# Kernel tuning notes

Hardware: AMD Instinct MI355X
Metric: run time of the kernel (lower is better)

Reference implementation:

```python
import jax, jax.numpy as jnp
import numpy as np

B, H, W = 8, 64, 64
D = 256          # in_dim == key_dim == value_dim
HEADS = 8
DK = D // HEADS  # per-head channels (key == value)
EPS = 1e-5


def _ln(x, g, b):
    m = jnp.mean(x, axis=-1, keepdims=True)
    v = jnp.var(x, axis=-1, keepdims=True)
    return (x - m) * jax.lax.rsqrt(v + EPS) * g + b


def setup_inputs() -> dict:
    key = jax.random.key(0)
    ks = jax.random.split(key, 8)
    return {
        "x1": jax.random.normal(ks[0], (B, H, W, 2 * D), jnp.float32),
        "x2": jax.random.normal(ks[1], (B, H, W, D), jnp.float32),
        "linear_w": jax.random.normal(ks[2], (2 * D, D), jnp.float32) * 0.02,
        "linear_b": jax.random.normal(ks[3], (D,), jnp.float32) * 0.02,
        "ln1_g": jnp.ones((D,), jnp.float32) + jax.random.normal(ks[4], (D,), jnp.float32) * 0.02,
        "ln1_b": jax.random.normal(ks[5], (D,), jnp.float32) * 0.02,
        "reproj_w": jax.random.normal(ks[6], (2 * D, D), jnp.float32) * 0.02,  # 1x1 conv kernel [out,in]
        "reproj_b": jax.random.normal(ks[7], (2 * D,), jnp.float32) * 0.02,
        "ln_attn_g": jnp.ones((2 * D,), jnp.float32),
        "ln_attn_b": jnp.zeros((2 * D,), jnp.float32),
    }


def _cross_attention(n1, n2, reproj_w, reproj_b, ln_g, ln_b):
    # n1 (values source), n2 (keys/queries source): [B,H,W,D]
    N = H * W
    v = n1.reshape(B, N, D).transpose(0, 2, 1).reshape(B, HEADS, DK, N)
    kq = n2.reshape(B, N, D).transpose(0, 2, 1).reshape(B, HEADS, DK, N)
    k = jax.nn.softmax(kq, axis=-1)  # softmax over tokens (dim=2 in torch slice)
    q = jax.nn.softmax(kq, axis=2)   # softmax over per-head channels (dim=1 in torch slice)
    # attended[b,h,d,n] = sum_m sum_e q[b,h,d,m] k[b,h,e,m] v[b,h,e,n]
    ctx = jnp.einsum('bhdm,bhem->bhde', q, k)          # [B,h,dk,dk]
    att = jnp.einsum('bhde,bhen->bhdn', ctx, v)        # [B,h,dk,N]
    agg = att.reshape(B, D, H, W)                      # concat heads along channels
    rep = jnp.einsum('od,bdhw->bohw', reproj_w, agg) + reproj_b[None, :, None, None]
    rep = rep.transpose(0, 2, 3, 1)                    # [B,H,W,2D]
    return _ln(rep, ln_g, ln_b)


def reference(x1, x2, linear_w, linear_b, ln1_g, ln1_b, reproj_w, reproj_b, ln_attn_g, ln_attn_b):
    n1 = _ln(x1 @ linear_w + linear_b, ln1_g, ln1_b)   # [B,H,W,D]
    n2 = _ln(x2, ln1_g, ln1_b)                          # [B,H,W,D]
    attn = _cross_attention(n1, n2, reproj_w, reproj_b, ln_attn_g, ln_attn_b)
    return x1 + attn
```

## Files before the change

kernel.cpp:

```cpp
#include <hip/hip_runtime.h>
#include <stdint.h>

typedef __bf16 bf16x8 __attribute__((ext_vector_type(8)));
typedef float f32x4 __attribute__((ext_vector_type(4)));

#define EPS 1e-5f

#define WAITVM(N) asm volatile("s_waitcnt vmcnt(" #N ")" ::: "memory")
#define WAITLGKM0 asm volatile("s_waitcnt lgkmcnt(0)" ::: "memory")

__device__ __forceinline__ void gl16(const void* g, void* l) {
    __builtin_amdgcn_global_load_lds(
        (const __attribute__((address_space(1))) unsigned int*)g,
        (__attribute__((address_space(3))) unsigned int*)l, 16, 0, 0);
}

__device__ __forceinline__ float b2f(unsigned short u) {
    union { unsigned int i; float f; } c; c.i = ((unsigned int)u) << 16; return c.f;
}
__device__ __forceinline__ unsigned short f2b(float f) {
    union { float f; unsigned int i; } c; c.f = f;
    unsigned int i = c.i;
    return (unsigned short)((i + 0x7FFFu + ((i >> 16) & 1u)) >> 16);
}

__global__ void k_zero(float* __restrict__ p, int n) {
    int i = blockIdx.x * 256 + threadIdx.x;
    if (i < n) p[i] = 0.0f;
}

__global__ void k_params(const float* __restrict__ lw, const float* __restrict__ rw,
                         const float* __restrict__ lb, const float* __restrict__ g1,
                         const float* __restrict__ b1, const float* __restrict__ rb,
                         const float* __restrict__ ga, const float* __restrict__ ba,
                         unsigned short* __restrict__ wt1,
                         unsigned short* __restrict__ rwb,
                         unsigned short* __restrict__ vec) {
    int gid = blockIdx.x * 256 + threadIdx.x;
    if (gid < 131072) {
        int k = gid >> 8, n = gid & 255;
        wt1[((size_t)(k >> 3) * 256 + n) * 8 + (k & 7)] = f2b(lw[gid]);
    } else if (gid < 262144) {
        int j = gid - 131072;
        rwb[j] = f2b(rw[j]);
    } else if (gid < 264448) {
        int j = gid - 262144;
        if (j < 256)       vec[j] = f2b(lb[j]);
        else if (j < 512)  vec[j] = f2b(g1[j - 256]);
        else if (j < 768)  vec[j] = f2b(b1[j - 512]);
        else if (j < 1280) vec[j] = f2b(rb[j - 768]);
        else if (j < 1792) vec[j] = f2b(ga[j - 1280]);
        else               vec[j] = f2b(ba[j - 1792]);
    }
}

__global__ __launch_bounds__(256) void k_stats(const float* __restrict__ x2,
                                               float2* __restrict__ stats) {
    int t = threadIdx.x, lane = t & 63, w = t >> 6;
    size_t row = (size_t)blockIdx.x * 4 + w;
    float4 f = *(const float4*)(x2 + row * 256 + lane * 4);
    float s = f.x + f.y + f.z + f.w;
    float q = f.x * f.x + f.y * f.y + f.z * f.z + f.w * f.w;
#pragma unroll
    for (int msk = 1; msk < 64; msk <<= 1) {
        s += __shfl_xor(s, msk, 64);
        q += __shfl_xor(q, msk, 64);
    }
    float mn = s * (1.0f / 256.0f);
    float rstd = rsqrtf(q * (1.0f / 256.0f) - mn * mn + EPS);
    if (lane == 0) stats[row] = make_float2(mn, rstd);
}

__global__ __launch_bounds__(256) void k_ctx(const float* __restrict__ x2,
                                             const float2* __restrict__ stats,
                                             const unsigned short* __restrict__ vec,
                                             float* __restrict__ ctxraw) {
    __shared__ float E[64 * 36];
    __shared__ float Q[64 * 36];
    __shared__ float gs[32], bs[32];
    int bh = blockIdx.x >> 3;
    int b = bh >> 3, h = bh & 7;
    int ch = blockIdx.x & 7;
    int t = threadIdx.x;
    if (t < 32) { gs[t] = b2f(vec[256 + h * 32 + t]); bs[t] = b2f(vec[512 + h * 32 + t]); }
    __syncthreads();
    int d = t >> 3, e0 = (t & 7) * 4;
    float a0 = 0.f, a1 = 0.f, a2 = 0.f, a3 = 0.f;
    const float* base = x2 + ((size_t)b * 4096 + ch * 512) * 256 + h * 32;
    int srow = b * 4096 + ch * 512;
    const int m = t >> 2, c0 = (t & 3) * 8;
    for (int s0 = 0; s0 < 512; s0 += 64) {
        float2 st = stats[srow + s0 + m];
        const float4* p = (const float4*)(base + (size_t)(s0 + m) * 256 + c0);
        float4 f0 = p[0], f1 = p[1];
        float ev[8];
        ev[0] = __expf((f0.x - st.x) * st.y * gs[c0 + 0] + bs[c0 + 0]);
        ev[1] = __expf((f0.y - st.x) * st.y * gs[c0 + 1] + bs[c0 + 1]);
        ev[2] = __expf((f0.z - st.x) * st.y * gs[c0 + 2] + bs[c0 + 2]);
        ev[3] = __expf((f0.w - st.x) * st.y * gs[c0 + 3] + bs[c0 + 3]);
        ev[4] = __expf((f1.x - st.x) * st.y * gs[c0 + 4] + bs[c0 + 4]);
        ev[5] = __expf((f1.y - st.x) * st.y * gs[c0 + 5] + bs[c0 + 5]);
        ev[6] = __expf((f1.z - st.x) * st.y * gs[c0 + 6] + bs[c0 + 6]);
        ev[7] = __expf((f1.w - st.x) * st.y * gs[c0 + 7] + bs[c0 + 7]);
        float ps = ev[0] + ev[1] + ev[2] + ev[3] + ev[4] + ev[5] + ev[6] + ev[7];
        ps += __shfl_xor(ps, 1, 64);
        ps += __shfl_xor(ps, 2, 64);
        float qi = 1.0f / ps;
        *(float4*)(E + m * 36 + c0)     = make_float4(ev[0], ev[1], ev[2], ev[3]);
        *(float4*)(E + m * 36 + c0 + 4) = make_float4(ev[4], ev[5], ev[6], ev[7]);
        *(float4*)(Q + m * 36 + c0)     = make_float4(ev[0]*qi, ev[1]*qi, ev[2]*qi, ev[3]*qi);
        *(float4*)(Q + m * 36 + c0 + 4) = make_float4(ev[4]*qi, ev[5]*qi, ev[6]*qi, ev[7]*qi);
        __syncthreads();
#pragma unroll 4
        for (int mm = 0; mm < 64; mm++) {
            float qd = Q[mm * 36 + d];
            float4 e4 = *(const float4*)(E + mm * 36 + e0);
            a0 += qd * e4.x; a1 += qd * e4.y; a2 += qd * e4.z; a3 += qd * e4.w;
        }
        __syncthreads();
    }
    float* dst = ctxraw + ((size_t)bh << 10) + (d << 5) + e0;
    atomicAdd(dst + 0, a0);
    atomicAdd(dst + 1, a1);
    atomicAdd(dst + 2, a2);
    atomicAdd(dst + 3, a3);
}

__global__ __launch_bounds__(256) void k_w2(const float* __restrict__ ctxraw,
                                            const unsigned short* __restrict__ rwb,
                                            unsigned short* __restrict__ w2t) {
    __shared__ float ctx_s[1024];
    __shared__ float cinv[32];
    int blk = blockIdx.x;
    int b = blk >> 6, h = (blk >> 3) & 7, os = blk & 7;
    int bh = b * 8 + h;
    int t = threadIdx.x;
#pragma unroll
    for (int i = 0; i < 4; i++) ctx_s[t + 256 * i] = ctxraw[((size_t)bh << 10) + t + 256 * i];
    __syncthreads();
    if (t < 32) {
        float s = 0.f;
#pragma unroll
        for (int d = 0; d < 32; d++) s += ctx_s[d * 32 + t];
        cinv[t] = 1.0f / s;
    }
    __syncthreads();
    int o = os * 64 + (t >> 2);
    int e0 = (t & 3) * 8;
    float wv[32];
    const uint4* wp = (const uint4*)(rwb + (size_t)o * 256 + h * 32);
#pragma unroll
    for (int qd = 0; qd < 4; qd++) {
        uint4 u = wp[qd];
        unsigned int uu[4] = {u.x, u.y, u.z, u.w};
#pragma unroll
        for (int j = 0; j < 4; j++) {
            wv[qd * 8 + j * 2]     = b2f((unsigned short)(uu[j] & 0xFFFFu));
            wv[qd * 8 + j * 2 + 1] = b2f((unsigned short)(uu[j] >> 16));
        }
    }
    float s[8];
#pragma unroll
    for (int j = 0; j < 8; j++) s[j] = 0.f;
#pragma unroll 8
    for (int d = 0; d < 32; d++) {
        float w = wv[d];
#pragma unroll
        for (int j = 0; j < 8; j++) s[j] += ctx_s[d * 32 + e0 + j] * w;
    }
    ushort4 o4a, o4b;
    o4a.x = f2b(s[0] * cinv[e0 + 0]); o4a.y = f2b(s[1] * cinv[e0 + 1]);
    o4a.z = f2b(s[2] * cinv[e0 + 2]); o4a.w = f2b(s[3] * cinv[e0 + 3]);
    o4b.x = f2b(s[4] * cinv[e0 + 4]); o4b.y = f2b(s[5] * cinv[e0 + 5]);
    o4b.z = f2b(s[6] * cinv[e0 + 6]); o4b.w = f2b(s[7] * cinv[e0 + 7]);
    int kb = h * 4 + (e0 >> 3);
    unsigned short* dst = w2t + (size_t)b * 131072 + ((size_t)kb * 512 + o) * 8;
    *(ushort4*)dst = o4a;
    *(ushort4*)(dst + 4) = o4b;
}

__global__ __launch_bounds__(256) void k_gemm1(
    const float* __restrict__ x1, const unsigned short* __restrict__ wt1,
    const unsigned short* __restrict__ vec, unsigned short* __restrict__ n1) {
    __shared__ __align__(16) char pool[33792];
    const int t = threadIdx.x;
    const int lane = t & 63, w = t >> 6;
    const int l15 = lane & 15, quad = lane >> 4;
    const int rb = blockIdx.x;
    const int row0 = rb * 64;
    const int mrow = (w << 4) + l15;

    const float* xrow = x1 + (size_t)(row0 + mrow) * 512 + quad * 8;

    f32x4 acc[16];
#pragma unroll
    for (int i = 0; i < 16; i++) acc[i] = (f32x4){0.f, 0.f, 0.f, 0.f};

    float4 fa[2][2];
    fa[0][0] = *(const float4*)(xrow);
    fa[0][1] = *(const float4*)(xrow + 4);
#pragma unroll
    for (int i = 0; i < 4; i++)
        gl16((const char*)wt1 + (w * 4 + i) * 1024 + lane * 16,
             pool + (w * 4 + i) * 1024);

#pragma unroll
    for (int s = 0; s < 16; ++s) {
        const int cur = s & 1;
        if (s < 15) {
            const float* xn = xrow + (s + 1) * 32;
            fa[cur ^ 1][0] = *(const float4*)xn;
            fa[cur ^ 1][1] = *(const float4*)(xn + 4);
#pragma unroll
            for (int i = 0; i < 4; i++)
                gl16((const char*)wt1 + (size_t)(s + 1) * 16384 + (w * 4 + i) * 1024 + lane * 16,
                     pool + (cur ^ 1) * 16384 + (w * 4 + i) * 1024);
        }
        bf16x8 af;
        af[0] = (__bf16)fa[cur][0].x; af[1] = (__bf16)fa[cur][0].y;
        af[2] = (__bf16)fa[cur][0].z; af[3] = (__bf16)fa[cur][0].w;
        af[4] = (__bf16)fa[cur][1].x; af[5] = (__bf16)fa[cur][1].y;
        af[6] = (__bf16)fa[cur][1].z; af[7] = (__bf16)fa[cur][1].w;
        if (s < 15) { WAITVM(6); } else { WAITVM(0); }
        __builtin_amdgcn_s_barrier();
        const char* Bc = pool + cur * 16384 + quad * 4096 + l15 * 16;
#pragma unroll
        for (int cb = 0; cb < 16; cb++) {
            bf16x8 bf = *(const bf16x8*)(Bc + cb * 256);
            acc[cb] = __builtin_amdgcn_mfma_f32_16x16x32_bf16(af, bf, acc[cb], 0, 0, 0);
        }
        WAITLGKM0;
        __builtin_amdgcn_s_barrier();
    }
#pragma unroll
    for (int cb = 0; cb < 16; cb++) {
        float bc = b2f(vec[(cb << 4) + l15]);
#pragma unroll
        for (int r = 0; r < 4; r++) acc[cb][r] += bc;
    }
    float mean_[4], rstd_[4];
#pragma unroll
    for (int r = 0; r < 4; r++) {
        float s = 0.f, q = 0.f;
#pragma unroll
        for (int cb = 0; cb < 16; cb++) { float v = acc[cb][r]; s += v; q += v * v; }
#pragma unroll
        for (int msk = 1; msk < 16; msk <<= 1) {
            s += __shfl_xor(s, msk, 64);
            q += __shfl_xor(q, msk, 64);
        }
        float mn = s * (1.0f / 256.0f);
        mean_[r] = mn;
        rstd_[r] = rsqrtf(q * (1.0f / 256.0f) - mn * mn + EPS);
    }
    unsigned short* n1s = (unsigned short*)pool;
#pragma unroll
    for (int cb = 0; cb < 16; cb++) {
        int col = (cb << 4) + l15;
        float gg = b2f(vec[256 + col]), bbv = b2f(vec[512 + col]);
#pragma unroll
        for (int r = 0; r < 4; r++) {
            int rr = (w << 4) + (quad << 2) + r;
            n1s[rr * 264 + col] = f2b((acc[cb][r] - mean_[r]) * rstd_[r] * gg + bbv);
        }
    }
    WAITLGKM0;
    __builtin_amdgcn_s_barrier();
    {
        int r = t >> 2;
        const unsigned short* src = n1s + r * 264;
        unsigned short* dst = n1 + (size_t)rb * 16384 + r * 8;
#pragma unroll
        for (int j = 0; j < 8; j++) {
            int chunk = (t & 3) * 8 + j;
            *(uint4*)(dst + chunk * 512) = *(const uint4*)(src + chunk * 8);
        }
    }
}

__global__ __launch_bounds__(512) void k_gemm2(
    const unsigned short* __restrict__ n1, const unsigned short* __restrict__ w2t,
    const unsigned short* __restrict__ vec, const float* __restrict__ x1,
    float* __restrict__ out) {
    __shared__ __align__(16) char pool[66560];
    __shared__ float2 red2[128];
    const int t = threadIdx.x;
    const int lane = t & 63, w = t >> 6;
    const int l15 = lane & 15, quad = lane >> 4;
    const int hf = w >> 2, wr = w & 3;
    const int rb = blockIdx.x;
    const int row0 = rb * 64;
    const char* wb = (const char*)w2t + (size_t)(rb >> 6) * 262144;
    const char* an = (const char*)n1 + (size_t)rb * 32768 + quad * 1024 + ((wr << 4) + l15) * 16;

    f32x4 acc[16];
#pragma unroll
    for (int i = 0; i < 16; i++) acc[i] = (f32x4){0.f, 0.f, 0.f, 0.f};

    bf16x8 areg[2];
    areg[0] = *(const bf16x8*)(an);
#pragma unroll
    for (int i = 0; i < 4; i++)
        gl16(wb + (w * 4 + i) * 1024 + lane * 16, pool + (w * 4 + i) * 1024);

#pragma unroll
    for (int s = 0; s < 8; ++s) {
        const int cur = s & 1;
        if (s < 7) {
            areg[cur ^ 1] = *(const bf16x8*)(an + (s + 1) * 4096);
#pragma unroll
            for (int i = 0; i < 4; i++)
                gl16(wb + (size_t)(s + 1) * 32768 + (w * 4 + i) * 1024 + lane * 16,
                     pool + (cur ^ 1) * 32768 + (w * 4 + i) * 1024);
            WAITVM(5);
        } else {
            WAITVM(0);
        }
        __builtin_amdgcn_s_barrier();
        const char* Bc = pool + cur * 32768 + quad * 8192 + hf * 4096 + l15 * 16;
#pragma unroll
        for (int cb = 0; cb < 16; cb++) {
            bf16x8 bf = *(const bf16x8*)(Bc + cb * 256);
            acc[cb] = __builtin_amdgcn_mfma_f32_16x16x32_bf16(areg[cur], bf, acc[cb], 0, 0, 0);
        }
        WAITLGKM0;
        __builtin_amdgcn_s_barrier();
    }
#pragma unroll
    for (int cb = 0; cb < 16; cb++) {
        float bc = b2f(vec[768 + (hf << 8) + (cb << 4) + l15]);
#pragma unroll
        for (int r = 0; r < 4; r++) acc[cb][r] += bc;
    }
#pragma unroll
    for (int r = 0; r < 4; r++) {
        float s = 0.f, q = 0.f;
#pragma unroll
        for (int cb = 0; cb < 16; cb++) { float v = acc[cb][r]; s += v; q += v * v; }
#pragma unroll
        for (int msk = 1; msk < 16; msk <<= 1) {
            s += __shfl_xor(s, msk, 64);
            q += __shfl_xor(q, msk, 64);
        }
        if (l15 == 0) red2[hf * 64 + (wr << 4) + (quad << 2) + r] = make_float2(s, q);
    }
    WAITLGKM0;
    __builtin_amdgcn_s_barrier();
    float mean_[4], rstd_[4];
#pragma unroll
    for (int r = 0; r < 4; r++) {
        int rl = (wr << 4) + (quad << 2) + r;
        float2 cA = red2[rl], cB = red2[64 + rl];
        float s = cA.x + cB.x, q = cA.y + cB.y;
        float mn = s * (1.0f / 512.0f);
        mean_[r] = mn;
        rstd_[r] = rsqrtf(q * (1.0f / 512.0f) - mn * mn + EPS);
    }
    float* rep = (float*)pool;
#pragma unroll
    for (int hv = 0; hv < 2; ++hv) {
        if (hv) __builtin_amdgcn_s_barrier();
        if (hf == hv) {
#pragma unroll
            for (int cb = 0; cb < 16; cb++) {
                int col = (cb << 4) + l15;
                int gcol = (hv << 8) + col;
                float gg = b2f(vec[1280 + gcol]), bbv = b2f(vec[1792 + gcol]);
#pragma unroll
                for (int r = 0; r < 4; r++)
                    rep[((wr << 4) + (quad << 2) + r) * 260 + col] =
                        (acc[cb][r] - mean_[r]) * rstd_[r] * gg + bbv;
            }
        }
        WAITLGKM0;
        __builtin_amdgcn_s_barrier();
        int rr = t >> 4, c0 = (t & 15) << 2;
#pragma unroll
        for (int j = 0; j < 4; j++) {
            int col = c0 + (j << 6);
            float4 v0 = *(const float4*)(rep + rr * 260 + col);
            float4 v1 = *(const float4*)(rep + (rr + 32) * 260 + col);
            size_t g0 = (size_t)(row0 + rr) * 512 + (hv << 8) + col;
            size_t g1 = g0 + (size_t)32 * 512;
            float4 xa = *(const float4*)(x1 + g0);
            float4 xb = *(const float4*)(x1 + g1);
            v0.x += xa.x; v0.y += xa.y; v0.z += xa.z; v0.w += xa.w;
            v1.x += xb.x; v1.y += xb.y; v1.z += xb.z; v1.w += xb.w;
            *(float4*)(out + g0) = v0;
            *(float4*)(out + g1) = v1;
        }
        WAITLGKM0;
    }
}

extern "C" void kernel_launch(void* const* d_in, const int* in_sizes, int n_in,
                              void* d_out, int out_size, void* d_ws, size_t ws_size,
                              hipStream_t stream) {
    const float* x1 = (const float*)d_in[0];
    const float* x2 = (const float*)d_in[1];
    const float* lw = (const float*)d_in[2];
    const float* lb = (const float*)d_in[3];
    const float* g1 = (const float*)d_in[4];
    const float* b1 = (const float*)d_in[5];
    const float* rw = (const float*)d_in[6];
    const float* rb = (const float*)d_in[7];
    const float* ga = (const float*)d_in[8];
    const float* ba = (const float*)d_in[9];
    float* out = (float*)d_out;

    char* ws = (char*)d_ws;
    float*          ctxr  = (float*)(ws);
    float2*         stats = (float2*)(ws + 262144);
    unsigned short* wt1   = (unsigned short*)(ws + 524288);
    unsigned short* rwb   = (unsigned short*)(ws + 786432);
    unsigned short* vec   = (unsigned short*)(ws + 1048576);
    unsigned short* w2t   = (unsigned short*)(ws + 1064960);
    unsigned short* n1    = (unsigned short*)(ws + 4194304);

    k_zero<<<dim3(256), dim3(256), 0, stream>>>(ctxr, 65536);
    k_params<<<dim3(1033), dim3(256), 0, stream>>>(lw, rw, lb, g1, b1, rb, ga, ba,
                                                   wt1, rwb, vec);
    k_stats<<<dim3(8192), dim3(256), 0, stream>>>(x2, stats);
    k_ctx<<<dim3(512), dim3(256), 0, stream>>>(x2, stats, vec, ctxr);
    k_w2<<<dim3(512), dim3(256), 0, stream>>>(ctxr, rwb, w2t);
    k_gemm1<<<dim3(512), dim3(256), 0, stream>>>(x1, wt1, vec, n1);
    k_gemm2<<<dim3(512), dim3(512), 0, stream>>>(n1, w2t, vec, x1, out);
}
```

Before: 234.6 us.

## Fuse linear+LN GEMM with reprojection GEMM into one kernel keeping n1 in LDS

Merges k_gemm1 and k_gemm2 into a single kernel that processes 128 rows per block with 512 threads, keeping the normalized n1 tile in shared memory instead of writing it to and re-reading it from global memory. Each wave now computes all 512 output columns (32 accumulators), which removes the cross-wave LayerNorm reduction. The second GEMM's first weight tile is prefetched while the first GEMM's epilogue runs. The cost is 130KB of dynamic LDS, one block per CU, only 256 blocks, and higher register pressure from 32 accumulator tiles.

```diff
diff --git a/kernel.cpp b/kernel.cpp
--- a/kernel.cpp
+++ b/kernel.cpp
@@ -179,30 +179,35 @@
     *(ushort4*)(dst + 4) = o4b;
 }
 
-__global__ __launch_bounds__(256) void k_gemm1(
+__global__ __launch_bounds__(512, 1) void k_fused(
     const float* __restrict__ x1, const unsigned short* __restrict__ wt1,
-    const unsigned short* __restrict__ vec, unsigned short* __restrict__ n1) {
-    __shared__ __align__(16) char pool[33792];
+    const unsigned short* __restrict__ w2t, const unsigned short* __restrict__ vec,
+    float* __restrict__ out) {
+    extern __shared__ __align__(16) char pool[];
+    unsigned short* n1s = (unsigned short*)pool;
+    char* Breg = pool + 67584;
+
     const int t = threadIdx.x;
     const int lane = t & 63, w = t >> 6;
     const int l15 = lane & 15, quad = lane >> 4;
     const int rb = blockIdx.x;
-    const int row0 = rb * 64;
-    const int mrow = (w << 4) + l15;
-
-    const float* xrow = x1 + (size_t)(row0 + mrow) * 512 + quad * 8;
+    const int row0 = rb << 7;
+    const char* wt1c = (const char*)wt1;
+    const char* wbase = (const char*)w2t + (size_t)(rb >> 5) * 262144;
+
+    const float* xrow = x1 + (size_t)(row0 + (w << 4) + l15) * 512 + quad * 8;
 
     f32x4 acc[16];
 #pragma unroll
     for (int i = 0; i < 16; i++) acc[i] = (f32x4){0.f, 0.f, 0.f, 0.f};
 
+#pragma unroll
+    for (int i = 0; i < 2; i++)
+        gl16(wt1c + ((w * 2 + i) << 10) + lane * 16,
+             Breg + ((w * 2 + i) << 10) + lane * 16);
     float4 fa[2][2];
-    fa[0][0] = *(const float4*)(xrow);
+    fa[0][0] = *(const float4*)xrow;
     fa[0][1] = *(const float4*)(xrow + 4);
-#pragma unroll
-    for (int i = 0; i < 4; i++)
-        gl16((const char*)wt1 + (w * 4 + i) * 1024 + lane * 16,
-             pool + (w * 4 + i) * 1024);
 
 #pragma unroll
     for (int s = 0; s < 16; ++s) {
@@ -212,18 +217,18 @@
             fa[cur ^ 1][0] = *(const float4*)xn;
             fa[cur ^ 1][1] = *(const float4*)(xn + 4);
 #pragma unroll
-            for (int i = 0; i < 4; i++)
-                gl16((const char*)wt1 + (size_t)(s + 1) * 16384 + (w * 4 + i) * 1024 + lane * 16,
-                     pool + (cur ^ 1) * 16384 + (w * 4 + i) * 1024);
+            for (int i = 0; i < 2; i++)
+                gl16(wt1c + (size_t)(s + 1) * 16384 + ((w * 2 + i) << 10) + lane * 16,
+                     Breg + (cur ^ 1) * 16384 + ((w * 2 + i) << 10) + lane * 16);
         }
         bf16x8 af;
         af[0] = (__bf16)fa[cur][0].x; af[1] = (__bf16)fa[cur][0].y;
         af[2] = (__bf16)fa[cur][0].z; af[3] = (__bf16)fa[cur][0].w;
         af[4] = (__bf16)fa[cur][1].x; af[5] = (__bf16)fa[cur][1].y;
         af[6] = (__bf16)fa[cur][1].z; af[7] = (__bf16)fa[cur][1].w;
-        if (s < 15) { WAITVM(6); } else { WAITVM(0); }
-        __builtin_amdgcn_s_barrier();
-        const char* Bc = pool + cur * 16384 + quad * 4096 + l15 * 16;
+        if (s < 15) { WAITVM(4); } else { WAITVM(0); }
+        __builtin_amdgcn_s_barrier();
+        const char* Bc = Breg + cur * 16384 + quad * 4096 + l15 * 16;
 #pragma unroll
         for (int cb = 0; cb < 16; cb++) {
             bf16x8 bf = *(const bf16x8*)(Bc + cb * 256);
@@ -232,11 +237,24 @@
         WAITLGKM0;
         __builtin_amdgcn_s_barrier();
     }
+
+    float bc_[16], gg_[16], bb_[16];
 #pragma unroll
     for (int cb = 0; cb < 16; cb++) {
-        float bc = b2f(vec[(cb << 4) + l15]);
-#pragma unroll
-        for (int r = 0; r < 4; r++) acc[cb][r] += bc;
+        int col = (cb << 4) + l15;
+        bc_[cb] = b2f(vec[col]);
+        gg_[cb] = b2f(vec[256 + col]);
+        bb_[cb] = b2f(vec[512 + col]);
+    }
+#pragma unroll
+    for (int i = 0; i < 4; i++)
+        gl16(wbase + ((w * 4 + i) << 10) + lane * 16,
+             Breg + 32768 + ((w * 4 + i) << 10) + lane * 16);
+
+#pragma unroll
+    for (int cb = 0; cb < 16; cb++) {
+#pragma unroll
+        for (int r = 0; r < 4; r++) acc[cb][r] += bc_[cb];
     }
     float mean_[4], rstd_[4];
 #pragma unroll
@@ -253,134 +271,94 @@
         mean_[r] = mn;
         rstd_[r] = rsqrtf(q * (1.0f / 256.0f) - mn * mn + EPS);
     }
-    unsigned short* n1s = (unsigned short*)pool;
 #pragma unroll
     for (int cb = 0; cb < 16; cb++) {
         int col = (cb << 4) + l15;
-        float gg = b2f(vec[256 + col]), bbv = b2f(vec[512 + col]);
 #pragma unroll
         for (int r = 0; r < 4; r++) {
             int rr = (w << 4) + (quad << 2) + r;
-            n1s[rr * 264 + col] = f2b((acc[cb][r] - mean_[r]) * rstd_[r] * gg + bbv);
+            n1s[rr * 264 + col] =
+                f2b((acc[cb][r] - mean_[r]) * rstd_[r] * gg_[cb] + bb_[cb]);
         }
     }
     WAITLGKM0;
     __builtin_amdgcn_s_barrier();
-    {
-        int r = t >> 2;
-        const unsigned short* src = n1s + r * 264;
-        unsigned short* dst = n1 + (size_t)rb * 16384 + r * 8;
-#pragma unroll
-        for (int j = 0; j < 8; j++) {
-            int chunk = (t & 3) * 8 + j;
-            *(uint4*)(dst + chunk * 512) = *(const uint4*)(src + chunk * 8);
-        }
-    }
-}
-
-__global__ __launch_bounds__(512) void k_gemm2(
-    const unsigned short* __restrict__ n1, const unsigned short* __restrict__ w2t,
-    const unsigned short* __restrict__ vec, const float* __restrict__ x1,
-    float* __restrict__ out) {
-    __shared__ __align__(16) char pool[66560];
-    __shared__ float2 red2[128];
-    const int t = threadIdx.x;
-    const int lane = t & 63, w = t >> 6;
-    const int l15 = lane & 15, quad = lane >> 4;
-    const int hf = w >> 2, wr = w & 3;
-    const int rb = blockIdx.x;
-    const int row0 = rb * 64;
-    const char* wb = (const char*)w2t + (size_t)(rb >> 6) * 262144;
-    const char* an = (const char*)n1 + (size_t)rb * 32768 + quad * 1024 + ((wr << 4) + l15) * 16;
-
-    f32x4 acc[16];
-#pragma unroll
-    for (int i = 0; i < 16; i++) acc[i] = (f32x4){0.f, 0.f, 0.f, 0.f};
-
-    bf16x8 areg[2];
-    areg[0] = *(const bf16x8*)(an);
-#pragma unroll
-    for (int i = 0; i < 4; i++)
-        gl16(wb + (w * 4 + i) * 1024 + lane * 16, pool + (w * 4 + i) * 1024);
+
+    f32x4 acc2[32];
+#pragma unroll
+    for (int i = 0; i < 32; i++) acc2[i] = (f32x4){0.f, 0.f, 0.f, 0.f};
+    const unsigned short* an1 = n1s + ((w << 4) + l15) * 264 + quad * 8;
 
 #pragma unroll
     for (int s = 0; s < 8; ++s) {
-        const int cur = s & 1;
+        const char* bufc = Breg + ((s & 1) ? 0 : 32768);
         if (s < 7) {
-            areg[cur ^ 1] = *(const bf16x8*)(an + (s + 1) * 4096);
+            char* bufn = Breg + (((s + 1) & 1) ? 0 : 32768);
 #pragma unroll
             for (int i = 0; i < 4; i++)
-                gl16(wb + (size_t)(s + 1) * 32768 + (w * 4 + i) * 1024 + lane * 16,
-                     pool + (cur ^ 1) * 32768 + (w * 4 + i) * 1024);
-            WAITVM(5);
-        } else {
-            WAITVM(0);
-        }
-        __builtin_amdgcn_s_barrier();
-        const char* Bc = pool + cur * 32768 + quad * 8192 + hf * 4096 + l15 * 16;
-#pragma unroll
-        for (int cb = 0; cb < 16; cb++) {
+                gl16(wbase + (size_t)(s + 1) * 32768 + ((w * 4 + i) << 10) + lane * 16,
+                     bufn + ((w * 4 + i) << 10) + lane * 16);
+        }
+        bf16x8 a2 = *(const bf16x8*)(an1 + s * 32);
+        if (s < 7) { WAITVM(4); } else { WAITVM(0); }
+        __builtin_amdgcn_s_barrier();
+        const char* Bc = bufc + quad * 8192 + l15 * 16;
+#pragma unroll
+        for (int cb = 0; cb < 32; cb++) {
             bf16x8 bf = *(const bf16x8*)(Bc + cb * 256);
-            acc[cb] = __builtin_amdgcn_mfma_f32_16x16x32_bf16(areg[cur], bf, acc[cb], 0, 0, 0);
+            acc2[cb] = __builtin_amdgcn_mfma_f32_16x16x32_bf16(a2, bf, acc2[cb], 0, 0, 0);
         }
         WAITLGKM0;
         __builtin_amdgcn_s_barrier();
     }
-#pragma unroll
-    for (int cb = 0; cb < 16; cb++) {
-        float bc = b2f(vec[768 + (hf << 8) + (cb << 4) + l15]);
-#pragma unroll
-        for (int r = 0; r < 4; r++) acc[cb][r] += bc;
-    }
+
+#pragma unroll
+    for (int cb = 0; cb < 32; cb++) {
+        float bc = b2f(vec[768 + (cb << 4) + l15]);
+#pragma unroll
+        for (int r = 0; r < 4; r++) acc2[cb][r] += bc;
+    }
+    float mean2[4], rstd2[4];
 #pragma unroll
     for (int r = 0; r < 4; r++) {
         float s = 0.f, q = 0.f;
 #pragma unroll
-        for (int cb = 0; cb < 16; cb++) { float v = acc[cb][r]; s += v; q += v * v; }
+        for (int cb = 0; cb < 32; cb++) { float v = acc2[cb][r]; s += v; q += v * v; }
 #pragma unroll
         for (int msk = 1; msk < 16; msk <<= 1) {
             s += __shfl_xor(s, msk, 64);
             q += __shfl_xor(q, msk, 64);
         }
-        if (l15 == 0) red2[hf * 64 + (wr << 4) + (quad << 2) + r] = make_float2(s, q);
-    }
-    WAITLGKM0;
-    __builtin_amdgcn_s_barrier();
-    float mean_[4], rstd_[4];
-#pragma unroll
-    for (int r = 0; r < 4; r++) {
-        int rl = (wr << 4) + (quad << 2) + r;
-        float2 cA = red2[rl], cB = red2[64 + rl];
-        float s = cA.x + cB.x, q = cA.y + cB.y;
         float mn = s * (1.0f / 512.0f);
-        mean_[r] = mn;
-        rstd_[r] = rsqrtf(q * (1.0f / 512.0f) - mn * mn + EPS);
+        mean2[r] = mn;
+        rstd2[r] = rsqrtf(q * (1.0f / 512.0f) - mn * mn + EPS);
     }
     float* rep = (float*)pool;
+    const int hfw = w >> 2;
 #pragma unroll
     for (int hv = 0; hv < 2; ++hv) {
         if (hv) __builtin_amdgcn_s_barrier();
-        if (hf == hv) {
-#pragma unroll
-            for (int cb = 0; cb < 16; cb++) {
+        if (hfw == hv) {
+#pragma unroll
+            for (int cb = 0; cb < 32; cb++) {
                 int col = (cb << 4) + l15;
-                int gcol = (hv << 8) + col;
-                float gg = b2f(vec[1280 + gcol]), bbv = b2f(vec[1792 + gcol]);
+                float gg = b2f(vec[1280 + col]), bbv = b2f(vec[1792 + col]);
+                int rl = ((w & 3) << 4) + (quad << 2);
 #pragma unroll
                 for (int r = 0; r < 4; r++)
-                    rep[((wr << 4) + (quad << 2) + r) * 260 + col] =
-                        (acc[cb][r] - mean_[r]) * rstd_[r] * gg + bbv;
+                    rep[(rl + r) * 516 + col] =
+                        (acc2[cb][r] - mean2[r]) * rstd2[r] * gg + bbv;
             }
         }
         WAITLGKM0;
         __builtin_amdgcn_s_barrier();
         int rr = t >> 4, c0 = (t & 15) << 2;
 #pragma unroll
-        for (int j = 0; j < 4; j++) {
+        for (int j = 0; j < 8; j++) {
             int col = c0 + (j << 6);
-            float4 v0 = *(const float4*)(rep + rr * 260 + col);
-            float4 v1 = *(const float4*)(rep + (rr + 32) * 260 + col);
-            size_t g0 = (size_t)(row0 + rr) * 512 + (hv << 8) + col;
+            float4 v0 = *(const float4*)(rep + rr * 516 + col);
+            float4 v1 = *(const float4*)(rep + (rr + 32) * 516 + col);
+            size_t g0 = (size_t)(row0 + (hv << 6) + rr) * 512 + col;
             size_t g1 = g0 + (size_t)32 * 512;
             float4 xa = *(const float4*)(x1 + g0);
             float4 xb = *(const float4*)(x1 + g1);
@@ -390,6 +368,7 @@
             *(float4*)(out + g1) = v1;
         }
         WAITLGKM0;
+        __builtin_amdgcn_s_barrier();
     }
 }
 
@@ -415,7 +394,13 @@
     unsigned short* rwb   = (unsigned short*)(ws + 786432);
     unsigned short* vec   = (unsigned short*)(ws + 1048576);
     unsigned short* w2t   = (unsigned short*)(ws + 1064960);
-    unsigned short* n1    = (unsigned short*)(ws + 4194304);
+
+    static bool attr_set = false;
+    if (!attr_set) {
+        hipFuncSetAttribute((const void*)k_fused,
+                            hipFuncAttributeMaxDynamicSharedMemorySize, 133120);
+        attr_set = true;
+    }
 
     k_zero<<<dim3(256), dim3(256), 0, stream>>>(ctxr, 65536);
     k_params<<<dim3(1033), dim3(256), 0, stream>>>(lw, rw, lb, g1, b1, rb, ga, ba,
@@ -423,6 +408,5 @@
     k_stats<<<dim3(8192), dim3(256), 0, stream>>>(x2, stats);
     k_ctx<<<dim3(512), dim3(256), 0, stream>>>(x2, stats, vec, ctxr);
     k_w2<<<dim3(512), dim3(256), 0, stream>>>(ctxr, rwb, w2t);
-    k_gemm1<<<dim3(512), dim3(256), 0, stream>>>(x1, wt1, vec, n1);
-    k_gemm2<<<dim3(512), dim3(512), 0, stream>>>(n1, w2t, vec, x1, out);
-}
+    k_fused<<<dim3(256), dim3(512), 133120, stream>>>(x1, wt1, w2t, vec, out);
+}
```

Result: faster. 228.8 us (-2.5%).
